# Kernel tuning notes

Hardware: AMD Instinct MI355X
Metric: run time of the kernel (lower is better)

The kernel has to match this reference:

```python
import jax, jax.numpy as jnp
import numpy as np

D_MODEL = 2048
N_HEADS = 16
HEAD_DIM = D_MODEL // N_HEADS


def setup_inputs() -> dict:
    key = jax.random.key(0)
    ks = jax.random.split(key, 5)
    s = 0.02
    return {
        "x": jax.random.normal(ks[0], (4, 2048, D_MODEL), dtype=jnp.float32),
        "w_qkv": jax.random.normal(ks[1], (D_MODEL, 3 * D_MODEL), dtype=jnp.float32) * s,
        "b_qkv": jnp.zeros((3 * D_MODEL,), dtype=jnp.float32),
        "w_out": jax.random.normal(ks[2], (D_MODEL, D_MODEL), dtype=jnp.float32) * s,
        "b_out": jnp.zeros((D_MODEL,), dtype=jnp.float32),
    }


def reference(x, w_qkv, b_qkv, w_out, b_out):
    B, T, C = x.shape
    qkv = x @ w_qkv + b_qkv  # [B,T,3C]
    q, k, v = jnp.split(qkv, 3, axis=-1)
    # [B,T,C] -> [B,H,T,hd]
    def to_heads(t):
        return t.reshape(B, T, N_HEADS, HEAD_DIM).transpose(0, 2, 1, 3)
    q, k, v = to_heads(q), to_heads(k), to_heads(v)
    scale = 1.0 / jnp.sqrt(jnp.asarray(HEAD_DIM, dtype=x.dtype))
    attn = jnp.einsum("bhqd,bhkd->bhqk", q, k) * scale
    causal = jnp.tril(jnp.ones((T, T), dtype=bool))
    attn = jnp.where(causal[None, None], attn, jnp.asarray(-jnp.inf, dtype=attn.dtype))
    attn = jax.nn.softmax(attn, axis=-1)
    out = jnp.einsum("bhqk,bhkd->bhqd", attn, v)
    out = out.transpose(0, 2, 1, 3).reshape(B, T, C)
    return out @ w_out + b_out
```

## Files before the change

### kernel.cpp

```cpp
#include <hip/hip_runtime.h>
#include <hip/hip_bf16.h>

#define DEVFN static __device__ __forceinline__

typedef __attribute__((ext_vector_type(8))) __bf16 bf16x8;
typedef __attribute__((ext_vector_type(4))) float f32x4;

#define MFMA16(a, b, c) __builtin_amdgcn_mfma_f32_16x16x32_bf16(a, b, c, 0, 0, 0)

DEVFN void gload16(const void* g, void* l) {
  __builtin_amdgcn_global_load_lds((const __attribute__((address_space(1))) void*)g,
                                   (__attribute__((address_space(3))) void*)l, 16, 0, 0);
}

DEVFN void vwait8() { asm volatile("s_waitcnt vmcnt(8)" ::: "memory"); __builtin_amdgcn_sched_barrier(0); }
DEVFN void vwait4() { asm volatile("s_waitcnt vmcnt(4)" ::: "memory"); __builtin_amdgcn_sched_barrier(0); }
DEVFN void vwait0() { asm volatile("s_waitcnt vmcnt(0)" ::: "memory"); __builtin_amdgcn_sched_barrier(0); }
DEVFN void bar()    { __builtin_amdgcn_s_barrier(); }
DEVFN void barsched() { __builtin_amdgcn_s_barrier(); __builtin_amdgcn_sched_barrier(0); }

__global__ __launch_bounds__(256) void cvt_f32_bf16(const float* __restrict__ in,
                                                    __bf16* __restrict__ out) {
  size_t i = ((size_t)blockIdx.x * 256 + threadIdx.x) * 8;
  f32x4 a = *(const f32x4*)(in + i);
  f32x4 b = *(const f32x4*)(in + i + 4);
  bf16x8 u;
  u[0] = (__bf16)a[0]; u[1] = (__bf16)a[1]; u[2] = (__bf16)a[2]; u[3] = (__bf16)a[3];
  u[4] = (__bf16)b[0]; u[5] = (__bf16)b[1]; u[6] = (__bf16)b[2]; u[7] = (__bf16)b[3];
  *(bf16x8*)(out + i) = u;
}

__global__ __launch_bounds__(256) void transpose_w(const float* __restrict__ in,
                                                   __bf16* __restrict__ out,
                                                   int K, int N) {
  __shared__ float tile[32][33];
  const int t = threadIdx.x, tx = t & 31, ty = t >> 5;
  const int n0 = blockIdx.x * 32, k0 = blockIdx.y * 32;
#pragma unroll
  for (int r = 0; r < 4; r++)
    tile[ty + r * 8][tx] = in[(size_t)(k0 + ty + r * 8) * N + n0 + tx];
  __syncthreads();
#pragma unroll
  for (int r = 0; r < 4; r++)
    out[(size_t)(n0 + ty + r * 8) * K + k0 + tx] = (__bf16)tile[tx][ty + r * 8];
}

__global__ __launch_bounds__(256) void transpose_v(const __bf16* __restrict__ in,
                                                   __bf16* __restrict__ out) {
  __shared__ __bf16 tile[64][72];
  const int bh = blockIdx.z;
  const int t0 = blockIdx.x * 64, d0 = blockIdx.y * 64;
  const int tid = threadIdx.x;
  const int r = tid >> 3, c8 = (tid & 7) * 8;
  const __bf16* ip = in + (size_t)bh * 2048 * 128;
#pragma unroll
  for (int i = 0; i < 2; i++)
    *(bf16x8*)&tile[i * 32 + r][c8] =
        *(const bf16x8*)(ip + (size_t)(t0 + i * 32 + r) * 128 + d0 + c8);
  __syncthreads();
  __bf16* op = out + (size_t)bh * 2048 * 128;
#pragma unroll
  for (int i = 0; i < 2; i++) {
    const int dd = i * 32 + r;
    bf16x8 v;
#pragma unroll
    for (int j = 0; j < 8; j++) v[j] = tile[c8 + j][dd];
    *(bf16x8*)(op + (size_t)(d0 + dd) * 2048 + t0 + c8) = v;
  }
}

#define QK_SCALE 0.12751745f

DEVFN void stage_tile(const __bf16* gx, size_t Kst, int t, __bf16* ldst,
                      int rr, int gsw, int w) {
#pragma unroll
  for (int j = 0; j < 4; j++)
    gload16(gx + (size_t)(j * 64 + rr) * Kst + (size_t)t * 64 + gsw,
            ldst + j * 4096 + w * 512);
}

DEVFN void tile_step(__bf16* la, __bf16* lb, f32x4 (&acc)[8][4],
                     const __bf16* ga, const __bf16* gb, size_t Kst, int t, int NT,
                     int rr, int gsw, int w, int wr, int wc, int lg, int li) {
  bf16x8 a[4][2], bl[2][2], br[2][2];
  const int sa = li & 7;
  const int arow = wr * 128 + li;
  const int brow = wc * 64 + li;
  const bool pf = (t + 2 < NT);

#pragma unroll
  for (int mi = 0; mi < 4; mi++)
#pragma unroll
    for (int ks = 0; ks < 2; ks++)
      a[mi][ks] = *(const bf16x8*)&la[(arow + mi * 16) * 64 + (((ks * 4 + lg) ^ sa) * 8)];
#pragma unroll
  for (int ni = 0; ni < 2; ni++)
#pragma unroll
    for (int ks = 0; ks < 2; ks++)
      bl[ni][ks] = *(const bf16x8*)&lb[(brow + ni * 16) * 64 + (((ks * 4 + lg) ^ sa) * 8)];
  bar();
  __builtin_amdgcn_s_setprio(1);
#pragma unroll
  for (int mi = 0; mi < 4; mi++)
#pragma unroll
    for (int ni = 0; ni < 2; ni++)
#pragma unroll
      for (int ks = 0; ks < 2; ks++)
        acc[mi][ni] = MFMA16(a[mi][ks], bl[ni][ks], acc[mi][ni]);
  __builtin_amdgcn_s_setprio(0);
  bar();

#pragma unroll
  for (int ni = 0; ni < 2; ni++)
#pragma unroll
    for (int ks = 0; ks < 2; ks++)
      br[ni][ks] = *(const bf16x8*)&lb[(brow + (ni + 2) * 16) * 64 + (((ks * 4 + lg) ^ sa) * 8)];
  bar();
  __builtin_amdgcn_s_setprio(1);
#pragma unroll
  for (int mi = 0; mi < 4; mi++)
#pragma unroll
    for (int ni = 0; ni < 2; ni++)
#pragma unroll
      for (int ks = 0; ks < 2; ks++)
        acc[mi][ni + 2] = MFMA16(a[mi][ks], br[ni][ks], acc[mi][ni + 2]);
  __builtin_amdgcn_s_setprio(0);
  barsched();

  if (pf) stage_tile(gb, Kst, t + 2, lb, rr, gsw, w);
#pragma unroll
  for (int mi = 0; mi < 4; mi++)
#pragma unroll
    for (int ks = 0; ks < 2; ks++)
      a[mi][ks] = *(const bf16x8*)&la[(arow + (mi + 4) * 16) * 64 + (((ks * 4 + lg) ^ sa) * 8)];
  bar();
  __builtin_amdgcn_s_setprio(1);
#pragma unroll
  for (int mi = 0; mi < 4; mi++)
#pragma unroll
    for (int ni = 0; ni < 2; ni++)
#pragma unroll
      for (int ks = 0; ks < 2; ks++)
        acc[mi + 4][ni] = MFMA16(a[mi][ks], bl[ni][ks], acc[mi + 4][ni]);
  __builtin_amdgcn_s_setprio(0);
  barsched();

  if (pf) stage_tile(ga, Kst, t + 2, la, rr, gsw, w);
  __builtin_amdgcn_s_setprio(1);
#pragma unroll
  for (int mi = 0; mi < 4; mi++)
#pragma unroll
    for (int ni = 0; ni < 2; ni++)
#pragma unroll
      for (int ks = 0; ks < 2; ks++)
        acc[mi + 4][ni + 2] = MFMA16(a[mi][ks], br[ni][ks], acc[mi + 4][ni + 2]);
  __builtin_amdgcn_s_setprio(0);

  if (pf) vwait8(); else vwait0();
  bar();
}

template <int MODE>
__global__ __launch_bounds__(512, 2) void gemm256(
    const __bf16* __restrict__ A, const __bf16* __restrict__ Bt,
    const float* __restrict__ bias, int K, int Ncols,
    __bf16* __restrict__ qo, __bf16* __restrict__ ko, __bf16* __restrict__ vo,
    float* __restrict__ outf) {
  __shared__ __align__(16) __bf16 lds[65536];
  const int tid = threadIdx.x;
  const int w = tid >> 6, lane = tid & 63;
  const int wr = w >> 2, wc = w & 3;
  const int lg = lane >> 4, li = lane & 15;
  const int nbx = gridDim.x;
  const int nwg = nbx * gridDim.y;
  const int orig = blockIdx.y * nbx + blockIdx.x;
  const int swz = (orig & 7) * (nwg >> 3) + (orig >> 3);
  const size_t m0 = (size_t)(swz / nbx) * 256;
  const size_t n0 = (size_t)(swz % nbx) * 256;
  const int rr = tid >> 3;
  const int gsw = ((tid & 7) ^ (rr & 7)) * 8;
  const __bf16* ga = A + m0 * K;
  const __bf16* gb = Bt + n0 * K;
  const int NT = K >> 6;

  __bf16* la0 = lds;
  __bf16* la1 = lds + 16384;
  __bf16* lb0 = lds + 32768;
  __bf16* lb1 = lds + 49152;

  f32x4 acc[8][4] = {};

  stage_tile(ga, K, 0, la0, rr, gsw, w);
  stage_tile(gb, K, 0, lb0, rr, gsw, w);
  stage_tile(ga, K, 1, la1, rr, gsw, w);
  stage_tile(gb, K, 1, lb1, rr, gsw, w);
  vwait8();
  bar();

  for (int t = 0; t < NT; t += 2) {
    tile_step(la0, lb0, acc, ga, gb, K, t,     NT, rr, gsw, w, wr, wc, lg, li);
    tile_step(la1, lb1, acc, ga, gb, K, t + 1, NT, rr, gsw, w, wr, wc, lg, li);
  }

  if (MODE == 0) {
    const int which = (int)(n0 >> 11);
    const int b = (int)(m0 >> 11);
    __bf16* outp = (which == 0) ? qo : ((which == 1) ? ko : vo);
    const float scale = (which == 0) ? QK_SCALE : 1.0f;
#pragma unroll
    for (int ni = 0; ni < 4; ni++) {
      const int ncol = (int)n0 + wc * 64 + ni * 16 + li;
      const float bv = bias[ncol];
      const int h = (ncol & 2047) >> 7;
      const int d = ncol & 127;
      const size_t base = (size_t)(b * 16 + h) * (2048 * 128) + d;
#pragma unroll
      for (int mi = 0; mi < 8; mi++)
#pragma unroll
        for (int r = 0; r < 4; r++) {
          const int tt = ((int)m0 + wr * 128 + mi * 16 + lg * 4 + r) & 2047;
          outp[base + (size_t)tt * 128] = (__bf16)((acc[mi][ni][r] + bv) * scale);
        }
    }
  } else {
#pragma unroll
    for (int ni = 0; ni < 4; ni++) {
      const int ncol = (int)n0 + wc * 64 + ni * 16 + li;
      const float bv = bias[ncol];
#pragma unroll
      for (int mi = 0; mi < 8; mi++)
#pragma unroll
        for (int r = 0; r < 4; r++) {
          const size_t mrow = m0 + wr * 128 + mi * 16 + lg * 4 + r;
          outf[mrow * Ncols + ncol] = acc[mi][ni][r] + bv;
        }
    }
  }
}

DEVFN void attn_stageK(const __bf16* const (&ksrc)[4], int k0, __bf16* Kl, int w) {
#pragma unroll
  for (int i = 0; i < 4; i++)
    gload16(ksrc[i] + (size_t)k0 * 128, Kl + i * 2048 + w * 512);
}
DEVFN void attn_stageV(const __bf16* const (&vsrc)[4], int k0, __bf16* Vl, int w) {
#pragma unroll
  for (int i = 0; i < 4; i++)
    gload16(vsrc[i] + k0, Vl + i * 2048 + w * 512);
}

template <bool DIAG>
DEVFN void attn_tile(int kt, int n, int q0, int w, int lg, int li,
                     const __bf16* const (&ksrc)[4], const __bf16* const (&vsrc)[4],
                     __bf16* Kl, __bf16* Vl, __bf16* Pl,
                     const bf16x8 (&qf)[2][4], f32x4 (&o)[2][8],
                     float (&mrow)[2][4], float (&lrow)[2][4]) {
  const int k0 = kt * 64;
  const bool more = (kt + 1 < n);

  vwait4();
  barsched();

  f32x4 s[2][4] = {};
#pragma unroll
  for (int kk = 0; kk < 4; kk++) {
    bf16x8 bk[4];
#pragma unroll
    for (int ni = 0; ni < 4; ni++) {
      const int key = ni * 16 + li;
      bk[ni] = *(const bf16x8*)&Kl[key * 128 + ((kk * 32 + lg * 8) ^ ((key & 7) << 3))];
    }
#pragma unroll
    for (int mi = 0; mi < 2; mi++)
#pragma unroll
      for (int ni = 0; ni < 4; ni++)
        s[mi][ni] = MFMA16(qf[mi][kk], bk[ni], s[mi][ni]);
  }
  barsched();
  if (more) attn_stageK(ksrc, k0 + 64, Kl, w);

#pragma unroll
  for (int mi = 0; mi < 2; mi++) {
#pragma unroll
    for (int r = 0; r < 4; r++) {
      const int prow = w * 32 + mi * 16 + lg * 4 + r;
      float vals[4];
#pragma unroll
      for (int ni = 0; ni < 4; ni++) {
        float x = s[mi][ni][r];
        if (DIAG) {
          if ((k0 + ni * 16 + li) > (q0 + prow)) x = -1e30f;
        }
        vals[ni] = x;
      }
      float vmax = fmaxf(fmaxf(vals[0], vals[1]), fmaxf(vals[2], vals[3]));
      vmax = fmaxf(vmax, __shfl_xor(vmax, 1));
      vmax = fmaxf(vmax, __shfl_xor(vmax, 2));
      vmax = fmaxf(vmax, __shfl_xor(vmax, 4));
      vmax = fmaxf(vmax, __shfl_xor(vmax, 8));
      float mref = mrow[mi][r];
      if (vmax - mref > 8.0f) {
        const float sc = __builtin_amdgcn_exp2f(mref - vmax);
        lrow[mi][r] *= sc;
#pragma unroll
        for (int nd = 0; nd < 8; nd++) o[mi][nd][r] *= sc;
        mrow[mi][r] = vmax;
        mref = vmax;
      }
      float ps = 0.f;
#pragma unroll
      for (int ni = 0; ni < 4; ni++) {
        const float p = __builtin_amdgcn_exp2f(vals[ni] - mref);
        ps += p;
        Pl[prow * 72 + ni * 16 + li] = (__bf16)p;
      }
      ps += __shfl_xor(ps, 1);
      ps += __shfl_xor(ps, 2);
      ps += __shfl_xor(ps, 4);
      ps += __shfl_xor(ps, 8);
      lrow[mi][r] += ps;
    }
  }

  if (more) vwait4(); else vwait0();
  barsched();

#pragma unroll
  for (int kk = 0; kk < 2; kk++) {
    bf16x8 pf[2];
#pragma unroll
    for (int mi = 0; mi < 2; mi++)
      pf[mi] = *(const bf16x8*)&Pl[(w * 32 + mi * 16 + li) * 72 + kk * 32 + lg * 8];
#pragma unroll
    for (int nd = 0; nd < 8; nd++) {
      const int d = nd * 16 + li;
      const int swd = ((d ^ (d >> 3)) & 7) << 3;
      bf16x8 vf = *(const bf16x8*)&Vl[d * 64 + ((kk * 32 + lg * 8) ^ swd)];
#pragma unroll
      for (int mi = 0; mi < 2; mi++)
        o[mi][nd] = MFMA16(pf[mi], vf, o[mi][nd]);
    }
  }
  barsched();
  if (more) attn_stageV(vsrc, k0 + 64, Vl, w);
}

DEVFN void attn_run(int qt, int bh, int w, int lg, int li,
                    const __bf16* qp, __bf16* ob,
                    const __bf16* const (&ksrc)[4], const __bf16* const (&vsrc)[4],
                    __bf16* Kl, __bf16* Vl, __bf16* Pl) {
  const int q0 = qt * 128;
  bf16x8 qf[2][4];
#pragma unroll
  for (int mi = 0; mi < 2; mi++)
#pragma unroll
    for (int kk = 0; kk < 4; kk++)
      qf[mi][kk] = *(const bf16x8*)(qp + (size_t)(q0 + w * 32 + mi * 16 + li) * 128 + kk * 32 + lg * 8);

  f32x4 o[2][8] = {};
  float mrow[2][4], lrow[2][4];
#pragma unroll
  for (int mi = 0; mi < 2; mi++)
#pragma unroll
    for (int r = 0; r < 4; r++) { mrow[mi][r] = -1e30f; lrow[mi][r] = 0.f; }

  const int n = 2 * qt + 2;
  attn_stageK(ksrc, 0, Kl, w);
  attn_stageV(vsrc, 0, Vl, w);

  for (int kt = 0; kt < n - 2; kt++)
    attn_tile<false>(kt, n, q0, w, lg, li, ksrc, vsrc, Kl, Vl, Pl, qf, o, mrow, lrow);
  attn_tile<true>(n - 2, n, q0, w, lg, li, ksrc, vsrc, Kl, Vl, Pl, qf, o, mrow, lrow);
  attn_tile<true>(n - 1, n, q0, w, lg, li, ksrc, vsrc, Kl, Vl, Pl, qf, o, mrow, lrow);

  const int b = bh >> 4, h = bh & 15;
#pragma unroll
  for (int mi = 0; mi < 2; mi++) {
    float inv[4];
#pragma unroll
    for (int r = 0; r < 4; r++) inv[r] = 1.0f / lrow[mi][r];
#pragma unroll
    for (int nd = 0; nd < 8; nd++)
#pragma unroll
      for (int r = 0; r < 4; r++)
        ob[(size_t)(b * 2048 + q0 + w * 32 + mi * 16 + lg * 4 + r) * 2048 + h * 128 + nd * 16 + li]
            = (__bf16)(o[mi][nd][r] * inv[r]);
  }
}

__global__ __launch_bounds__(256, 2) void attn_fwd(
    const __bf16* __restrict__ qb, const __bf16* __restrict__ kb,
    const __bf16* __restrict__ vtb, __bf16* __restrict__ ob) {
  __shared__ __align__(16) __bf16 Kl[64 * 128];
  __shared__ __align__(16) __bf16 Vl[128 * 64];
  __shared__ __align__(16) __bf16 Pl[128 * 72];
  const int orig = (int)blockIdx.y * 8 + (int)blockIdx.x;
  const int swz = (orig & 7) * 64 + (orig >> 3);
  const int bx = swz & 7;
  const int bh = swz >> 3;
  const int tid = threadIdx.x;
  const int w = tid >> 6, l = tid & 63;
  const int lg = l >> 4, li = l & 15;
  const __bf16* qp = qb + (size_t)bh * (2048 * 128);
  const __bf16* kp = kb + (size_t)bh * (2048 * 128);
  const __bf16* vtp = vtb + (size_t)bh * (2048 * 128);

  const __bf16* ksrc[4];
  const __bf16* vsrc[4];
#pragma unroll
  for (int i = 0; i < 4; i++) {
    const int key = i * 16 + w * 4 + lg;
    ksrc[i] = kp + (size_t)key * 128 + 8 * (li ^ (key & 7));
    const int d = i * 32 + (tid >> 3);
    const int g = (tid & 7) ^ ((d ^ (d >> 3)) & 7);
    vsrc[i] = vtp + (size_t)d * 2048 + g * 8;
  }

  attn_run(15 - bx, bh, w, lg, li, qp, ob, ksrc, vsrc, Kl, Vl, Pl);
  attn_run(bx,      bh, w, lg, li, qp, ob, ksrc, vsrc, Kl, Vl, Pl);
}

extern "C" void kernel_launch(void* const* d_in, const int* in_sizes, int n_in,
                              void* d_out, int out_size, void* d_ws, size_t ws_size,
                              hipStream_t stream) {
  (void)in_sizes; (void)n_in; (void)out_size; (void)ws_size;
  const float* x     = (const float*)d_in[0];
  const float* w_qkv = (const float*)d_in[1];
  const float* b_qkv = (const float*)d_in[2];
  const float* w_out = (const float*)d_in[3];
  const float* b_out = (const float*)d_in[4];
  float* out = (float*)d_out;
  char* ws = (char*)d_ws;

  __bf16* xb    = (__bf16*)(ws + 0);
  __bf16* wqkvT = (__bf16*)(ws + 33554432);
  __bf16* qbuf  = (__bf16*)(ws + 58720256);
  __bf16* kbuf  = (__bf16*)(ws + 92274688);
  __bf16* vbuf  = (__bf16*)(ws + 125829120);
  __bf16* woutT = (__bf16*)(ws + 159383552);

  cvt_f32_bf16<<<8192, 256, 0, stream>>>(x, xb);
  transpose_w<<<dim3(192, 64), 256, 0, stream>>>(w_qkv, wqkvT, 2048, 6144);
  transpose_w<<<dim3(64, 64), 256, 0, stream>>>(w_out, woutT, 2048, 2048);
  gemm256<0><<<dim3(24, 32), 512, 0, stream>>>(xb, wqkvT, b_qkv, 2048, 6144,
                                               qbuf, kbuf, vbuf, nullptr);
  transpose_v<<<dim3(32, 2, 64), 256, 0, stream>>>(vbuf, xb);
  attn_fwd<<<dim3(8, 64), 256, 0, stream>>>(qbuf, kbuf, xb, vbuf);
  gemm256<1><<<dim3(8, 32), 512, 0, stream>>>(vbuf, woutT, b_out, 2048, 2048,
                                              nullptr, nullptr, nullptr, out);
}
```

Baseline: 452.5 us.

## Split tile prefetch into chunks and remap workgroups into XCD-local 8x4 bands

The GEMM main loop now issues the next-tile global-to-LDS prefetch in per-chunk pieces. The pieces are spread across the MFMA phases, each issued as soon as the LDS rows it overwrites have been read, instead of two whole-tile bursts. The workgroup-to-tile mapping is also replaced: instead of the simple mod-8 XCD interleave, each XCD gets a 2D region (8 row tiles by 4 column bands) to improve L2 reuse of A and B. The new mapping hardcodes assumptions about grid shape (multiples of 8 rows per XCD and 4-column bands), so it may mis-map or lose coverage for other grid sizes.

```diff
diff --git a/kernel.cpp b/kernel.cpp
--- a/kernel.cpp
+++ b/kernel.cpp
@@ -79,6 +79,12 @@
             ldst + j * 4096 + w * 512);
 }
 
+DEVFN void stage_chunk(const __bf16* gx, size_t Kst, int t, __bf16* ldst, int j,
+                       int rr, int gsw, int w) {
+  gload16(gx + (size_t)(j * 64 + rr) * Kst + (size_t)t * 64 + gsw,
+          ldst + j * 4096 + w * 512);
+}
+
 DEVFN void tile_step(__bf16* la, __bf16* lb, f32x4 (&acc)[8][4],
                      const __bf16* ga, const __bf16* gb, size_t Kst, int t, int NT,
                      int rr, int gsw, int w, int wr, int wc, int lg, int li) {
@@ -108,13 +114,17 @@
       for (int ks = 0; ks < 2; ks++)
         acc[mi][ni] = MFMA16(a[mi][ks], bl[ni][ks], acc[mi][ni]);
   __builtin_amdgcn_s_setprio(0);
-  bar();
+  barsched();
 
 #pragma unroll
   for (int ni = 0; ni < 2; ni++)
 #pragma unroll
     for (int ks = 0; ks < 2; ks++)
       br[ni][ks] = *(const bf16x8*)&lb[(brow + (ni + 2) * 16) * 64 + (((ks * 4 + lg) ^ sa) * 8)];
+  if (pf) {
+    stage_chunk(ga, Kst, t + 2, la, 0, rr, gsw, w);
+    stage_chunk(ga, Kst, t + 2, la, 2, rr, gsw, w);
+  }
   bar();
   __builtin_amdgcn_s_setprio(1);
 #pragma unroll
@@ -127,12 +137,15 @@
   __builtin_amdgcn_s_setprio(0);
   barsched();
 
-  if (pf) stage_tile(gb, Kst, t + 2, lb, rr, gsw, w);
 #pragma unroll
   for (int mi = 0; mi < 4; mi++)
 #pragma unroll
     for (int ks = 0; ks < 2; ks++)
       a[mi][ks] = *(const bf16x8*)&la[(arow + (mi + 4) * 16) * 64 + (((ks * 4 + lg) ^ sa) * 8)];
+  if (pf) {
+    stage_chunk(gb, Kst, t + 2, lb, 0, rr, gsw, w);
+    stage_chunk(gb, Kst, t + 2, lb, 1, rr, gsw, w);
+  }
   bar();
   __builtin_amdgcn_s_setprio(1);
 #pragma unroll
@@ -145,7 +158,12 @@
   __builtin_amdgcn_s_setprio(0);
   barsched();
 
-  if (pf) stage_tile(ga, Kst, t + 2, la, rr, gsw, w);
+  if (pf) {
+    stage_chunk(gb, Kst, t + 2, lb, 2, rr, gsw, w);
+    stage_chunk(gb, Kst, t + 2, lb, 3, rr, gsw, w);
+    stage_chunk(ga, Kst, t + 2, la, 1, rr, gsw, w);
+    stage_chunk(ga, Kst, t + 2, la, 3, rr, gsw, w);
+  }
   __builtin_amdgcn_s_setprio(1);
 #pragma unroll
   for (int mi = 0; mi < 4; mi++)
@@ -172,11 +190,14 @@
   const int wr = w >> 2, wc = w & 3;
   const int lg = lane >> 4, li = lane & 15;
   const int nbx = gridDim.x;
-  const int nwg = nbx * gridDim.y;
-  const int orig = blockIdx.y * nbx + blockIdx.x;
-  const int swz = (orig & 7) * (nwg >> 3) + (orig >> 3);
-  const size_t m0 = (size_t)(swz / nbx) * 256;
-  const size_t n0 = (size_t)(swz % nbx) * 256;
+  const int orig = (int)blockIdx.y * nbx + (int)blockIdx.x;
+  const int x = orig & 7, i = orig >> 3;
+  const int xc = x & 1, xr = x >> 1;
+  const int hw = nbx >> 1;
+  const int band = i >> 5;
+  const int j = i & 31;
+  const size_t n0 = (size_t)(xc * hw + band * 4 + (j & 3)) * 256;
+  const size_t m0 = (size_t)(xr * 8 + (j >> 2)) * 256;
   const int rr = tid >> 3;
   const int gsw = ((tid & 7) ^ (rr & 7)) * 8;
   const __bf16* ga = A + m0 * K;
```

Result: no change. 457.6 us (+1.1%).
